# Optimization experiments

Hardware: AMD Instinct MI355X
Metric: run time of the kernel (lower is better)

## Reference

```python
import jax, jax.numpy as jnp
import numpy as np

N = 50000
E = 1600000
D_IN = 128
D_OUT = 128


def setup_inputs() -> dict:
    key = jax.random.key(0)
    k1, k2, k3, k4 = jax.random.split(key, 4)
    x = jax.random.normal(k1, (N, D_IN), dtype=jnp.float32)
    edge_index = jax.random.randint(k2, (2, E), 0, N, dtype=jnp.int64)
    # Linear(in_channels, out_channels) params (torch layout: W [out, in])
    bound = 1.0 / np.sqrt(D_IN)
    W = jax.random.uniform(k3, (D_OUT, D_IN), minval=-bound, maxval=bound, dtype=jnp.float32)
    b = jax.random.uniform(k4, (D_OUT,), minval=-bound, maxval=bound, dtype=jnp.float32)
    return {"x": x, "edge_index": edge_index, "W": W, "b": b}


def reference(x, edge_index, W, b):
    src, dst = edge_index[0], edge_index[1]
    # degree of each node as a source: tg.utils.degree(edge_index[0])
    deg = jax.ops.segment_sum(jnp.ones((E,), dtype=x.dtype), src, num_segments=N)
    norm = jnp.sqrt(deg + 1.0)[:, None]  # [N, 1]
    xn = x / norm
    # message passing with self_loop=True: scatter-add into x itself (out=x)
    agg = xn + jax.ops.segment_sum(xn[src], dst, num_segments=N)  # [N, D_IN]
    h = agg / norm
    return h @ W.T + b
```

## Files before the change

kernel.cpp:

```cpp
#include <hip/hip_runtime.h>

#define NN 50000
#define NE 1600000
#define D 128
#define RPB 40
#define NR 2
#define RNG 25000
#define NC 32
#define CHUNK 50000
#define NC2 64
#define CHUNK2 25000
#define NB 49

#define WS_INV  0
#define WS_CNT  204800
#define WS_OFF  409600
#define WS_BSUM 610304
#define WS_WT   614400
#define WS_PDST 679936
#define WS_PSRC 13479936
#define WS_CSR  16679936
#define WS_XNB  679936

__global__ __launch_bounds__(1024) void fused_pre(const int* __restrict__ ei,
                                                  const float* __restrict__ W,
                                                  unsigned short* __restrict__ psrc,
                                                  int* __restrict__ pdst,
                                                  float* __restrict__ Wt) {
    __shared__ int h[RNG];
    int bid = blockIdx.x;
    if (bid < 64) {
        int r = bid >> 5, c = bid & 31;
        int lo = r * RNG;
        for (int j = threadIdx.x; j < RNG; j += 1024) h[j] = 0;
        __syncthreads();
        const int* s = ei + c * CHUNK;
        for (int i = threadIdx.x; i < CHUNK; i += 1024) {
            int k = s[i] - lo;
            if ((unsigned)k < RNG) atomicAdd(&h[k], 1);
        }
        __syncthreads();
        unsigned short* p = psrc + (size_t)bid * RNG;
        for (int j = threadIdx.x; j < RNG; j += 1024) p[j] = (unsigned short)h[j];
    } else if (bid < 192) {
        int b2 = bid - 64;
        int r = b2 >> 6, c = b2 & 63;
        int lo = r * RNG;
        for (int j = threadIdx.x; j < RNG; j += 1024) h[j] = 0;
        __syncthreads();
        const int* d = ei + NE + c * CHUNK2;
        for (int i = threadIdx.x; i < CHUNK2; i += 1024) {
            int k = d[i] - lo;
            if ((unsigned)k < RNG) atomicAdd(&h[k], 1);
        }
        __syncthreads();
        int* p = pdst + (size_t)b2 * RNG;
        for (int j = threadIdx.x; j < RNG; j += 1024) p[j] = h[j];
    } else {
        int i = (bid - 192) * 1024 + threadIdx.x;
        int c = i >> 7, k = i & 127;
        Wt[k * D + c] = W[i];
    }
}

__global__ void reduce_both(const unsigned short* __restrict__ psrc,
                            const int* __restrict__ pdst,
                            float* __restrict__ inv, int* __restrict__ cnt) {
    int k = blockIdx.x * blockDim.x + threadIdx.x;
    if (k >= NN) return;
    int r = k / RNG, j = k - r * RNG;
    size_t bs = (size_t)(r * NC) * RNG + j;
    int s = 0;
#pragma unroll 8
    for (int c = 0; c < NC; ++c) s += psrc[bs + (size_t)c * RNG];
    size_t bd = (size_t)(r * NC2) * RNG + j;
    int t = 0;
#pragma unroll 8
    for (int c = 0; c < NC2; ++c) t += pdst[bd + (size_t)c * RNG];
    inv[k] = rsqrtf((float)s + 1.0f);
    cnt[k] = t;
}

__global__ __launch_bounds__(1024) void scan_blocks(const int* __restrict__ cnt,
                                                    int* __restrict__ off,
                                                    int* __restrict__ bsum) {
    __shared__ int s[1024];
    int tid = threadIdx.x;
    int i = blockIdx.x * 1024 + tid;
    int v = (i < NN) ? cnt[i] : 0;
    s[tid] = v;
    __syncthreads();
    for (int d = 1; d < 1024; d <<= 1) {
        int t = (tid >= d) ? s[tid - d] : 0;
        __syncthreads();
        s[tid] += t;
        __syncthreads();
    }
    if (i < NN) off[i] = s[tid] - v;
    if (tid == 1023) bsum[blockIdx.x] = s[1023];
}

__global__ void scan_chunks(int* __restrict__ pdst, int* __restrict__ off,
                            const int* __restrict__ bsum) {
    int k = blockIdx.x * blockDim.x + threadIdx.x;
    if (k >= NN) return;
    int bi = k >> 10;
    int top = 0;
#pragma unroll 8
    for (int c = 0; c < bi; ++c) top += bsum[c];
    int run = off[k] + top;
    off[k] = run;
    int r = k / RNG, j = k - r * RNG;
    size_t base = (size_t)(r * NC2) * RNG + j;
#pragma unroll 8
    for (int c = 0; c < NC2; ++c) {
        size_t p = base + (size_t)c * RNG;
        int v = pdst[p];
        pdst[p] = run;
        run += v;
    }
}

__global__ __launch_bounds__(1024) void fill_sorted(const int* __restrict__ ei,
                                                    const int* __restrict__ bases,
                                                    unsigned short* __restrict__ csr) {
    __shared__ int cur[RNG];
    int r = blockIdx.x >> 6, c = blockIdx.x & 63;
    int lo = r * RNG;
    const int* bslice = bases + (size_t)blockIdx.x * RNG;
    for (int j = threadIdx.x; j < RNG; j += 1024) cur[j] = bslice[j];
    __syncthreads();
    const int* s = ei + c * CHUNK2;
    const int* d = ei + NE + c * CHUNK2;
    for (int i = threadIdx.x; i < CHUNK2; i += 1024) {
        int kd = d[i] - lo;
        if ((unsigned)kd < RNG) {
            int pos = atomicAdd(&cur[kd], 1);
            csr[pos] = (unsigned short)s[i];
        }
    }
}

__device__ __forceinline__ unsigned bf16_rne(float f) {
    unsigned u = __float_as_uint(f);
    return (u + 0x7fffu + ((u >> 16) & 1u)) >> 16;
}
__global__ void scale_kernel(const float* __restrict__ x, const float* __restrict__ inv,
                             unsigned* __restrict__ xnb4) {
    int i = blockIdx.x * blockDim.x + threadIdx.x;
    if (i >= NN * 16) return;
    int row = i >> 4;
    float w = inv[row];
    const float4* src = (const float4*)(x + (size_t)i * 8);
    float4 a = src[0], bq = src[1];
    uint4 o;
    o.x = bf16_rne(a.x * w)  | (bf16_rne(a.y * w) << 16);
    o.y = bf16_rne(a.z * w)  | (bf16_rne(a.w * w) << 16);
    o.z = bf16_rne(bq.x * w) | (bf16_rne(bq.y * w) << 16);
    o.w = bf16_rne(bq.z * w) | (bf16_rne(bq.w * w) << 16);
    ((uint4*)xnb4)[i] = o;
}

#define ACC2(u) do { \
    ax += __uint_as_float((u).x << 16); \
    ay += __uint_as_float((u).x & 0xffff0000u); \
    az += __uint_as_float((u).y << 16); \
    aw += __uint_as_float((u).y & 0xffff0000u); } while (0)

__global__ __launch_bounds__(256) void gather_kernel(const unsigned* __restrict__ xnb,
                                                     const float* __restrict__ inv,
                                                     const int* __restrict__ off,
                                                     const int* __restrict__ cnt,
                                                     const unsigned short* __restrict__ csr,
                                                     float* __restrict__ out) {
    int wid = (blockIdx.x * blockDim.x + threadIdx.x) >> 6;
    if (wid >= NN) return;
    int lane = threadIdx.x & 63;
    int half = lane >> 5;
    int col4 = lane & 31;

    float ax = 0.f, ay = 0.f, az = 0.f, aw = 0.f;
    const uint2* xb = (const uint2*)xnb;
    if (half == 0) {
        uint2 u = xb[(size_t)wid * 32 + col4];
        ACC2(u);
    }
    int n = cnt[wid];
    const unsigned short* row = csr + off[wid];
    int i = half;
    for (; i + 14 < n; i += 16) {
        int s0 = row[i],      s1 = row[i + 2],  s2 = row[i + 4],  s3 = row[i + 6];
        int s4 = row[i + 8],  s5 = row[i + 10], s6 = row[i + 12], s7 = row[i + 14];
        uint2 u0 = xb[(size_t)s0 * 32 + col4];
        uint2 u1 = xb[(size_t)s1 * 32 + col4];
        uint2 u2 = xb[(size_t)s2 * 32 + col4];
        uint2 u3 = xb[(size_t)s3 * 32 + col4];
        uint2 u4 = xb[(size_t)s4 * 32 + col4];
        uint2 u5 = xb[(size_t)s5 * 32 + col4];
        uint2 u6 = xb[(size_t)s6 * 32 + col4];
        uint2 u7 = xb[(size_t)s7 * 32 + col4];
        ACC2(u0); ACC2(u1); ACC2(u2); ACC2(u3);
        ACC2(u4); ACC2(u5); ACC2(u6); ACC2(u7);
    }
    for (; i + 6 < n; i += 8) {
        int s0 = row[i], s1 = row[i + 2], s2 = row[i + 4], s3 = row[i + 6];
        uint2 u0 = xb[(size_t)s0 * 32 + col4];
        uint2 u1 = xb[(size_t)s1 * 32 + col4];
        uint2 u2 = xb[(size_t)s2 * 32 + col4];
        uint2 u3 = xb[(size_t)s3 * 32 + col4];
        ACC2(u0); ACC2(u1); ACC2(u2); ACC2(u3);
    }
    for (; i < n; i += 2) {
        int s = row[i];
        uint2 u = xb[(size_t)s * 32 + col4];
        ACC2(u);
    }
    ax += __shfl_xor(ax, 32, 64);
    ay += __shfl_xor(ay, 32, 64);
    az += __shfl_xor(az, 32, 64);
    aw += __shfl_xor(aw, 32, 64);
    if (half == 0) {
        float wn = inv[wid];
        float4 o;
        o.x = ax * wn; o.y = ay * wn; o.z = az * wn; o.w = aw * wn;
        ((float4*)(out + (size_t)wid * D))[col4] = o;
    }
}

__global__ __launch_bounds__(256) void gemm_kernel(float* io, const float* __restrict__ Wt,
                                                   const float* __restrict__ b) {
    __shared__ float h[RPB][D];
    int r0 = blockIdx.x * RPB;

    const float4* src4 = (const float4*)(io + (size_t)r0 * D);
    for (int t = threadIdx.x; t < RPB * D / 4; t += 256) {
        ((float4*)h)[t] = src4[t];
    }
    __syncthreads();

    int c = threadIdx.x & 127;
    int rh = threadIdx.x >> 7;
    float acc[20];
#pragma unroll
    for (int j = 0; j < 20; ++j) acc[j] = 0.0f;

    for (int k0 = 0; k0 < D; k0 += 4) {
        float w0 = Wt[(k0 + 0) * D + c];
        float w1 = Wt[(k0 + 1) * D + c];
        float w2 = Wt[(k0 + 2) * D + c];
        float w3 = Wt[(k0 + 3) * D + c];
#pragma unroll
        for (int j = 0; j < 20; ++j) {
            float4 hv = *(const float4*)&h[rh * 20 + j][k0];
            acc[j] += hv.x * w0 + hv.y * w1 + hv.z * w2 + hv.w * w3;
        }
    }

    float bc = b[c];
#pragma unroll
    for (int j = 0; j < 20; ++j) {
        io[(size_t)(r0 + rh * 20 + j) * D + c] = acc[j] + bc;
    }
}

extern "C" void kernel_launch(void* const* d_in, const int* in_sizes, int n_in,
                              void* d_out, int out_size, void* d_ws, size_t ws_size,
                              hipStream_t stream) {
    const float* x  = (const float*)d_in[0];
    const int*   ei = (const int*)d_in[1];
    const float* W  = (const float*)d_in[2];
    const float* b  = (const float*)d_in[3];
    float* out = (float*)d_out;

    char* ws = (char*)d_ws;
    float*          inv  = (float*)         (ws + WS_INV);
    int*            cnt  = (int*)           (ws + WS_CNT);
    int*            off  = (int*)           (ws + WS_OFF);
    int*            bsum = (int*)           (ws + WS_BSUM);
    float*          Wt   = (float*)         (ws + WS_WT);
    int*            pdst = (int*)           (ws + WS_PDST);
    unsigned short* psrc = (unsigned short*)(ws + WS_PSRC);
    unsigned short* csr  = (unsigned short*)(ws + WS_CSR);
    unsigned*       xnb  = (unsigned*)      (ws + WS_XNB);

    fused_pre<<<208, 1024, 0, stream>>>(ei, W, psrc, pdst, Wt);
    reduce_both<<<(NN + 255) / 256, 256, 0, stream>>>(psrc, pdst, inv, cnt);
    scan_blocks<<<NB, 1024, 0, stream>>>(cnt, off, bsum);
    scan_chunks<<<(NN + 255) / 256, 256, 0, stream>>>(pdst, off, bsum);
    fill_sorted<<<NR * NC2, 1024, 0, stream>>>(ei, pdst, csr);
    scale_kernel<<<(NN * 16 + 255) / 256, 256, 0, stream>>>(x, inv, xnb);
    gather_kernel<<<(NN * 64 + 255) / 256, 256, 0, stream>>>(xnb, inv, off, cnt, csr, out);
    gemm_kernel<<<NN / RPB, 256, 0, stream>>>(out, Wt, b);
}
```

Baseline: 166.9 us.

## Split histogram node ranges into four and fuse reduction with block scan

Node ranges for the src/dst histograms shrink from 25000 to 12500, so twice as many blocks each use half the shared memory, which allows more occupancy and parallelism in the preprocessing kernels. The per-node partial reduction is merged with the block-level prefix scan into one kernel using 256-thread blocks, removing a launch and a re-read of the counts. The cost is that each histogram block re-reads its whole edge chunk for a smaller range, so global reads of edge_index double. The cross-block prefix loop in scan_chunks also grows to 196 block sums. Correctness depends on the unseen fill_sorted code and the workspace layout matching the new range split.

```diff
diff --git a/kernel.cpp b/kernel.cpp
--- a/kernel.cpp
+++ b/kernel.cpp
@@ -4,13 +4,13 @@
 #define NE 1600000
 #define D 128
 #define RPB 40
-#define NR 2
-#define RNG 25000
+#define NRS 4
+#define RNG 12500
 #define NC 32
 #define CHUNK 50000
 #define NC2 64
 #define CHUNK2 25000
-#define NB 49
+#define NBS 196
 
 #define WS_INV  0
 #define WS_CNT  204800
@@ -29,7 +29,7 @@
                                                   float* __restrict__ Wt) {
     __shared__ int h[RNG];
     int bid = blockIdx.x;
-    if (bid < 64) {
+    if (bid < 128) {
         int r = bid >> 5, c = bid & 31;
         int lo = r * RNG;
         for (int j = threadIdx.x; j < RNG; j += 1024) h[j] = 0;
@@ -42,8 +42,8 @@
         __syncthreads();
         unsigned short* p = psrc + (size_t)bid * RNG;
         for (int j = threadIdx.x; j < RNG; j += 1024) p[j] = (unsigned short)h[j];
-    } else if (bid < 192) {
-        int b2 = bid - 64;
+    } else if (bid < 384) {
+        int b2 = bid - 128;
         int r = b2 >> 6, c = b2 & 63;
         int lo = r * RNG;
         for (int j = threadIdx.x; j < RNG; j += 1024) h[j] = 0;
@@ -57,56 +57,52 @@
         int* p = pdst + (size_t)b2 * RNG;
         for (int j = threadIdx.x; j < RNG; j += 1024) p[j] = h[j];
     } else {
-        int i = (bid - 192) * 1024 + threadIdx.x;
+        int i = (bid - 384) * 1024 + threadIdx.x;
         int c = i >> 7, k = i & 127;
         Wt[k * D + c] = W[i];
     }
 }
 
-__global__ void reduce_both(const unsigned short* __restrict__ psrc,
-                            const int* __restrict__ pdst,
-                            float* __restrict__ inv, int* __restrict__ cnt) {
-    int k = blockIdx.x * blockDim.x + threadIdx.x;
-    if (k >= NN) return;
-    int r = k / RNG, j = k - r * RNG;
-    size_t bs = (size_t)(r * NC) * RNG + j;
-    int s = 0;
+__global__ __launch_bounds__(256) void reduce_scan(const unsigned short* __restrict__ psrc,
+                                                   const int* __restrict__ pdst,
+                                                   float* __restrict__ inv,
+                                                   int* __restrict__ cnt,
+                                                   int* __restrict__ off,
+                                                   int* __restrict__ bsum) {
+    __shared__ int sh[256];
+    int tid = threadIdx.x;
+    int k = blockIdx.x * 256 + tid;
+    int t = 0;
+    if (k < NN) {
+        int r = k / RNG, j = k - r * RNG;
+        size_t bs = (size_t)(r * NC) * RNG + j;
+        int s = 0;
 #pragma unroll 8
-    for (int c = 0; c < NC; ++c) s += psrc[bs + (size_t)c * RNG];
-    size_t bd = (size_t)(r * NC2) * RNG + j;
-    int t = 0;
+        for (int c = 0; c < NC; ++c) s += psrc[bs + (size_t)c * RNG];
+        size_t bd = (size_t)(r * NC2) * RNG + j;
 #pragma unroll 8
-    for (int c = 0; c < NC2; ++c) t += pdst[bd + (size_t)c * RNG];
-    inv[k] = rsqrtf((float)s + 1.0f);
-    cnt[k] = t;
-}
-
-__global__ __launch_bounds__(1024) void scan_blocks(const int* __restrict__ cnt,
-                                                    int* __restrict__ off,
-                                                    int* __restrict__ bsum) {
-    __shared__ int s[1024];
-    int tid = threadIdx.x;
-    int i = blockIdx.x * 1024 + tid;
-    int v = (i < NN) ? cnt[i] : 0;
-    s[tid] = v;
+        for (int c = 0; c < NC2; ++c) t += pdst[bd + (size_t)c * RNG];
+        inv[k] = rsqrtf((float)s + 1.0f);
+        cnt[k] = t;
+    }
+    sh[tid] = t;
     __syncthreads();
-    for (int d = 1; d < 1024; d <<= 1) {
-        int t = (tid >= d) ? s[tid - d] : 0;
-        __syncthreads();
-        s[tid] += t;
-        __syncthreads();
-    }
-    if (i < NN) off[i] = s[tid] - v;
-    if (tid == 1023) bsum[blockIdx.x] = s[1023];
+    for (int d = 1; d < 256; d <<= 1) {
+        int v = (tid >= d) ? sh[tid - d] : 0;
+        __syncthreads();
+        sh[tid] += v;
+        __syncthreads();
+    }
+    if (k < NN) off[k] = sh[tid] - t;
+    if (tid == 255) bsum[blockIdx.x] = sh[255];
 }
 
 __global__ void scan_chunks(int* __restrict__ pdst, int* __restrict__ off,
                             const int* __restrict__ bsum) {
     int k = blockIdx.x * blockDim.x + threadIdx.x;
     if (k >= NN) return;
-    int bi = k >> 10;
+    int bi = k >> 8;
     int top = 0;
-#pragma unroll 8
     for (int c = 0; c < bi; ++c) top += bsum[c];
     int run = off[k] + top;
     off[k] = run;
@@ -283,11 +279,10 @@
     unsigned short* csr  = (unsigned short*)(ws + WS_CSR);
     unsigned*       xnb  = (unsigned*)      (ws + WS_XNB);
 
-    fused_pre<<<208, 1024, 0, stream>>>(ei, W, psrc, pdst, Wt);
-    reduce_both<<<(NN + 255) / 256, 256, 0, stream>>>(psrc, pdst, inv, cnt);
-    scan_blocks<<<NB, 1024, 0, stream>>>(cnt, off, bsum);
+    fused_pre<<<400, 1024, 0, stream>>>(ei, W, psrc, pdst, Wt);
+    reduce_scan<<<NBS, 256, 0, stream>>>(psrc, pdst, inv, cnt, off, bsum);
     scan_chunks<<<(NN + 255) / 256, 256, 0, stream>>>(pdst, off, bsum);
-    fill_sorted<<<NR * NC2, 1024, 0, stream>>>(ei, pdst, csr);
+    fill_sorted<<<NRS * NC2, 1024, 0, stream>>>(ei, pdst, csr);
     scale_kernel<<<(NN * 16 + 255) / 256, 256, 0, stream>>>(x, inv, xnb);
     gather_kernel<<<(NN * 64 + 255) / 256, 256, 0, stream>>>(xnb, inv, off, cnt, csr, out);
     gemm_kernel<<<NN / RPB, 256, 0, stream>>>(out, Wt, b);
```

After: 164.7 us. No clear change (-1.4%).
